# Kernel tuning notes

Hardware: AMD Instinct MI355X
Metric: run time of the kernel (lower is better)

## Reference

```python
import jax, jax.numpy as jnp
import numpy as np

B, S, D = 4, 4096, 1024
G, N, BLK, K = 8, 64, 8, 4
GD = D // G
NL = 24


def setup_inputs() -> dict:
    key = jax.random.key(0)
    ks = jax.random.split(key, 16)
    f32 = jnp.float32
    rn = lambda k, sh, s: jax.random.normal(k, sh, f32) * s
    inp = {}
    inp["x_r"] = jax.random.normal(ks[0], (B, S, D), f32)
    inp["x_i"] = jax.random.normal(ks[1], (B, S, D), f32)
    inp["norm_w"] = jnp.ones((D,), f32)
    inp["sg_theta"] = rn(ks[2], (D // BLK,), 0.1)
    inp["sg_Wg"] = rn(ks[3], (D, D), 1.0 / np.sqrt(D))
    inp["sg_bg"] = jnp.zeros((D,), f32)
    inp["conv_w"] = rn(ks[4], (2 * D, 2, K), 1.0 / np.sqrt(2 * K))
    inp["conv_b"] = jnp.zeros((2 * D,), f32)
    inp["log_A_mag"] = jax.random.uniform(ks[5], (G, N), f32) * 0.5 + 0.5
    inp["A_phase"] = rn(ks[6], (G, N), 0.1)
    inp["B_Wr"] = rn(ks[7], (N, GD), 1.0 / np.sqrt(GD))
    inp["B_Wi"] = rn(ks[8], (N, GD), 1.0 / np.sqrt(GD))
    inp["C_Wr"] = rn(ks[9], (GD, N), 1.0 / np.sqrt(N))
    inp["C_Wi"] = rn(ks[10], (GD, N), 1.0 / np.sqrt(N))
    inp["dt_W"] = rn(ks[11], (2, 2 * GD), 1.0 / np.sqrt(2 * GD))
    inp["dt_b"] = jnp.zeros((2,), f32)
    inp["out_Wr"] = rn(ks[12], (D, D), 1.0 / np.sqrt(D))
    inp["out_Wi"] = rn(ks[13], (D, D), 1.0 / np.sqrt(D))
    inp["act_thr"] = jnp.zeros((), f32)
    inp["ssm_scale"] = jnp.full((D,), 2.5, f32)
    inp["res_scale"] = jnp.asarray(1.0 / np.sqrt(2.0 * NL), f32)
    return inp


def reference(x_r, x_i, norm_w, sg_theta, sg_Wg, sg_bg, conv_w, conv_b,
              log_A_mag, A_phase, B_Wr, B_Wi, C_Wr, C_Wi, dt_W, dt_b,
              out_Wr, out_Wi, act_thr, ssm_scale, res_scale):
    b, s, d = x_r.shape
    g, n, gd = G, N, GD
    # --- ComplexRMSNorm: normalize by RMS of complex magnitude ---
    inv = jax.lax.rsqrt(jnp.mean(x_r * x_r + x_i * x_i, axis=-1, keepdims=True) + 1e-6)
    xr = x_r * inv * norm_w
    xi = x_i * inv * norm_w
    # --- SpinorGate: block-diagonal phase rotation with selective sigmoid gate ---
    theta = jnp.repeat(sg_theta, BLK)  # per-block angle broadcast to [D]
    mag = jnp.sqrt(xr * xr + xi * xi + 1e-8)
    gate = jax.nn.sigmoid(jnp.einsum('bsd,ed->bse', mag, sg_Wg) + sg_bg)
    ct, st = jnp.cos(theta), jnp.sin(theta)
    xr, xi = gate * (xr * ct - xi * st), gate * (xr * st + xi * ct)
    # --- grouped causal conv over interleaved real/imag channels ---
    x_il = jnp.stack([xr, xi], axis=-1).reshape(b, s, 2 * d).transpose(0, 2, 1)  # [B,2D,S]
    x_il = jnp.pad(x_il, ((0, 0), (0, 0), (K - 1, 0)))  # causal left pad
    co = jax.lax.conv_general_dilated(
        x_il, conv_w, (1,), 'VALID',
        dimension_numbers=('NCH', 'OIH', 'NCH'), feature_group_count=d)
    co = co + conv_b[None, :, None]
    co = co.transpose(0, 2, 1).reshape(b, s, d, 2)
    xr, xi = co[..., 0], co[..., 1]
    # --- magnitude-gated activation ---
    act = 1.0 - jnp.exp(-(xr * xr + xi * xi) * jnp.exp(act_thr))
    xr = xr * act
    xi = xi * act
    # --- MIMO groups ---
    xgr = xr.reshape(b, s, g, gd)
    xgi = xi.reshape(b, s, g, gd)
    # --- selective dt from concatenated real/imag features ---
    xcat = jnp.concatenate([xgr, xgi], axis=-1)  # [B,S,G,2*gd]
    dt = jnp.clip(jnp.exp(jnp.einsum('bsgd,ed->bsge', xcat, dt_W) + dt_b), 1e-4, 2.0)
    dt_mag, dt_ph = dt[..., 0:1], dt[..., 1:2]
    # --- discretized complex A (|A| < 1 guaranteed) ---
    a_mag = jnp.exp(dt_mag * (-jax.nn.softplus(log_A_mag)))  # [B,S,G,N]
    ang = dt_ph * A_phase
    ar = a_mag * jnp.cos(ang)
    ai = a_mag * jnp.sin(ang)
    # --- complex B projection ---
    bxr = (jnp.einsum('bsgd,nd->bsgn', xgr, B_Wr)
           - jnp.einsum('bsgd,nd->bsgn', xgi, B_Wi)) * dt_mag
    bxi = (jnp.einsum('bsgd,nd->bsgn', xgr, B_Wi)
           + jnp.einsum('bsgd,nd->bsgn', xgi, B_Wr)) * dt_mag
    # --- complex selective scan with renorm every 256 steps ---
    def step(carry, inp):
        hr, hi = carry
        a_r, a_i, b_r, b_i, t = inp
        nhr = a_r * hr - a_i * hi + b_r
        nhi = a_r * hi + a_i * hr + b_i
        hn = jnp.sqrt(nhr * nhr + nhi * nhi + 1e-8)
        sc = jnp.where((t + 1) % 256 == 0, jnp.minimum(hn, 100.0) / hn, 1.0)
        nhr = nhr * sc
        nhi = nhi * sc
        return (nhr, nhi), (nhr, nhi)

    h0 = jnp.zeros((b, g, n), x_r.dtype)
    mv = lambda a: jnp.moveaxis(a, 1, 0)  # [S,B,G,N]
    _, (Hr, Hi) = jax.lax.scan(step, (h0, h0),
                               (mv(ar), mv(ai), mv(bxr), mv(bxi), jnp.arange(s)))
    Hr = jnp.moveaxis(Hr, 0, 1)  # [B,S,G,N]
    Hi = jnp.moveaxis(Hi, 0, 1)
    # --- complex C projection ---
    yr = (jnp.einsum('bsgn,dn->bsgd', Hr, C_Wr)
          - jnp.einsum('bsgn,dn->bsgd', Hi, C_Wi)).reshape(b, s, d)
    yi = (jnp.einsum('bsgn,dn->bsgd', Hr, C_Wi)
          + jnp.einsum('bsgn,dn->bsgd', Hi, C_Wr)).reshape(b, s, d)
    # --- complex output projection, real per-channel scale, residual ---
    o_r = (jnp.einsum('bsd,ed->bse', yr, out_Wr)
           - jnp.einsum('bsd,ed->bse', yi, out_Wi)) * ssm_scale
    o_i = (jnp.einsum('bsd,ed->bse', yr, out_Wi)
           + jnp.einsum('bsd,ed->bse', yi, out_Wr)) * ssm_scale
    return jnp.stack([x_r + res_scale * o_r, x_i + res_scale * o_i], axis=-1)
```

## Files before the change

### kernel.cpp

```cpp
#include <hip/hip_runtime.h>
#include <hip/hip_bf16.h>
#include <hip/hip_fp8.h>
#include <math.h>

#define BB 4
#define SS 4096
#define DD 1024
#define GG 8
#define NN 64
#define GDIM 128
#define BS (BB*SS)
static const size_t BSD  = (size_t)BS * DD;
static const size_t BSGN = (size_t)BS * GG * NN;

typedef __attribute__((ext_vector_type(8))) short bf16x8;
typedef __attribute__((ext_vector_type(4))) float f32x4;
typedef __attribute__((ext_vector_type(4))) uint u32x4;
typedef unsigned char uchar;

__device__ inline ushort f2b(float x) {
    __hip_bfloat16 h = __float2bfloat16(x);
    return *reinterpret_cast<ushort*>(&h);
}
__device__ inline float b2f(ushort u) {
    union { uint q; float f; } x; x.q = ((uint)u) << 16; return x.f;
}
__device__ inline uchar f2fp8(float x) {
    __hip_fp8_e4m3 h(x);
    return *reinterpret_cast<uchar*>(&h);
}
__device__ __forceinline__ bf16x8 neg8(bf16x8 v) {
    union { bf16x8 b; u32x4 u; } x;
    x.b = v;
    x.u ^= 0x80008000u;
    return x.b;
}

#define GL16(gp, lp) __builtin_amdgcn_global_load_lds( \
    (const __attribute__((address_space(1))) void*)(gp), \
    (__attribute__((address_space(3))) void*)(lp), 16, 0, 0)

template<int KD, int LDA, int LDB>
__device__ __forceinline__ void mfma_core(
    const ushort* __restrict__ gA, const ushort* __restrict__ gB,
    ushort* lA, ushort* lB, int wave, int lane, f32x4 (&acc)[4][4])
{
    int r = lane & 15, h = lane >> 4;
    int wm = (wave & 1) * 64, wn = (wave >> 1) * 64;
    ushort* lA0 = lA + wave * 1024;
    ushort* lB0 = lB + wave * 1024;
    for (int k0 = 0; k0 < KD; k0 += 32) {
        __syncthreads();
        GL16(gA + k0,            lA0);
        GL16(gA + k0 + 16*LDA,   lA0 + 512);
        GL16(gB + k0,            lB0);
        GL16(gB + k0 + 16*LDB,   lB0 + 512);
        __syncthreads();
        bf16x8 af[4], bfv[4];
        #pragma unroll
        for (int i = 0; i < 4; i++) af[i]  = *(const bf16x8*)&lA[(wm + i*16 + r)*32 + h*8];
        #pragma unroll
        for (int j = 0; j < 4; j++) bfv[j] = *(const bf16x8*)&lB[(wn + j*16 + r)*32 + h*8];
        #pragma unroll
        for (int i = 0; i < 4; i++)
            #pragma unroll
            for (int j = 0; j < 4; j++)
                acc[i][j] = __builtin_amdgcn_mfma_f32_16x16x32_bf16(af[i], bfv[j], acc[i][j], 0, 0, 0);
    }
}

__global__ __launch_bounds__(256) void k_prep(
    const float* __restrict__ Wg, const float* __restrict__ BWr, const float* __restrict__ BWi,
    const float* __restrict__ CWr, const float* __restrict__ CWi,
    const float* __restrict__ Wor, const float* __restrict__ Woi,
    const float* __restrict__ logA, const float* __restrict__ theta,
    uchar* __restrict__ Wg8, ushort* __restrict__ BxT, ushort* __restrict__ A3,
    ushort* __restrict__ WoP, float* __restrict__ spl,
    float* __restrict__ ctab, float* __restrict__ stab)
{
    const int S1 = 1048576;
    const int S2 = S1 + 32768;
    const int S3 = S2 + 32768;
    const int S4 = S3 + 2097152;
    const int S5 = S4 + 512;
    const int S6 = S5 + 1024;
    const int S7 = S6 + 1024;
    for (int idx = blockIdx.x * 256 + threadIdx.x; idx < S7; idx += gridDim.x * 256) {
        if (idx < S1) {
            Wg8[idx] = f2fp8(Wg[idx] * 16.0f);
        } else if (idx < S2) {
            int j = idx - S1, n = j >> 8, kk = j & 255;
            float v;
            if (n < 64) v = (kk < 128) ? BWr[n*128 + kk] : -BWi[n*128 + (kk-128)];
            else { int n2 = n - 64; v = (kk < 128) ? BWi[n2*128 + kk] : BWr[n2*128 + (kk-128)]; }
            BxT[j] = f2b(v);
        } else if (idx < S3) {
            int j = idx - S2, m = j >> 8, kk = j & 255;
            float v;
            if (m < 64) v = (kk < 128) ? CWr[kk*64 + m] : -CWi[(kk-128)*64 + m];
            else { int n2 = m - 64; v = (kk < 128) ? CWi[kk*64 + n2] : CWr[(kk-128)*64 + n2]; }
            A3[j] = f2b(v);
        } else if (idx < S4) {
            int j = idx - S3, e = j >> 11, c = j & 2047;
            int g = c >> 8, kk = c & 255;
            float v = (kk < 128) ? Wor[(size_t)e*1024 + g*128 + kk]
                                 : Woi[(size_t)e*1024 + g*128 + (kk-128)];
            WoP[j] = f2b(v);
        } else if (idx < S5) {
            int j = idx - S4;
            spl[j] = log1pf(expf(logA[j]));
        } else if (idx < S6) {
            int j = idx - S5;
            ctab[j] = cosf(theta[j >> 3]);
        } else {
            int j = idx - S6;
            stab[j] = sinf(theta[j >> 3]);
        }
    }
}

__global__ __launch_bounds__(256) void k_pgemm(
    const ushort* __restrict__ A3, const ushort* __restrict__ WoP,
    ushort* __restrict__ Ppr, ushort* __restrict__ Ppi)
{
    __shared__ ushort lA[4096], lB[4096];
    int g = blockIdx.z;
    int bn = blockIdx.x * 128;
    int tid = threadIdx.x, wave = tid >> 6, lane = tid & 63;
    int row0 = wave*32 + (lane >> 2), col0 = (lane & 3) * 8;
    int r = lane & 15, h = lane >> 4;
    int wm = (wave & 1) * 64, wn = (wave >> 1) * 64;
    f32x4 acc[4][4] = {};
    mfma_core<256, 256, 2048>(A3 + (size_t)row0*256 + col0,
                              WoP + (size_t)(bn + row0)*2048 + g*256 + col0,
                              lA, lB, wave, lane, acc);
    #pragma unroll
    for (int i = 0; i < 4; i++) {
        int mb = wm + i*16 + h*4;
        #pragma unroll
        for (int j = 0; j < 4; j++) {
            int e = bn + wn + j*16 + r;
            #pragma unroll
            for (int t2 = 0; t2 < 4; t2++) {
                int m = mb + t2;
                float v = acc[i][j][t2];
                if (m < 64) {
                    Ppr[(size_t)e*512 + g*64 + m] = f2b(v);
                } else {
                    Ppi[(size_t)e*512 + g*64 + (m - 64)] = f2b(v);
                }
            }
        }
    }
}

__global__ __launch_bounds__(256) void k_norm(
    const float* __restrict__ xr_in, const float* __restrict__ xi_in,
    const float* __restrict__ norm_w,
    uchar* __restrict__ mag_o, float* __restrict__ inv_o)
{
    int row = blockIdx.x;
    int tid = threadIdx.x;
    size_t base = (size_t)row * DD;
    float4 vr = ((const float4*)(xr_in + base))[tid];
    float4 vi = ((const float4*)(xi_in + base))[tid];
    float ss = vr.x*vr.x + vr.y*vr.y + vr.z*vr.z + vr.w*vr.w
             + vi.x*vi.x + vi.y*vi.y + vi.z*vi.z + vi.w*vi.w;
    #pragma unroll
    for (int off = 32; off >= 1; off >>= 1) ss += __shfl_down(ss, off);
    __shared__ float ws4[4];
    if ((tid & 63) == 0) ws4[tid >> 6] = ss;
    __syncthreads();
    float tot = ws4[0] + ws4[1] + ws4[2] + ws4[3];
    float inv = rsqrtf(tot * (1.0f / DD) + 1e-6f);
    float4 w = ((const float4*)norm_w)[tid];
    vr.x *= inv * w.x; vr.y *= inv * w.y; vr.z *= inv * w.z; vr.w *= inv * w.w;
    vi.x *= inv * w.x; vi.y *= inv * w.y; vi.z *= inv * w.z; vi.w *= inv * w.w;
    uchar4 mb;
    mb.x = f2fp8(sqrtf(vr.x*vr.x + vi.x*vi.x + 1e-8f));
    mb.y = f2fp8(sqrtf(vr.y*vr.y + vi.y*vi.y + 1e-8f));
    mb.z = f2fp8(sqrtf(vr.z*vr.z + vi.z*vi.z + 1e-8f));
    mb.w = f2fp8(sqrtf(vr.w*vr.w + vi.w*vi.w + 1e-8f));
    ((uchar4*)(mag_o + base))[tid] = mb;
    if (tid == 0) inv_o[row] = inv;
}

__global__ __launch_bounds__(256) void k_gate_fp8(
    const uchar* __restrict__ A8, const uchar* __restrict__ B8,
    const float* __restrict__ bg, ushort* __restrict__ gate)
{
    __shared__ uchar lA[4096], lB[4096];
    int flat = blockIdx.y * 8 + blockIdx.x;
    int nid  = (flat & 7) * 128 + (flat >> 3);
    int bm = (nid >> 3) * 128, bn = (nid & 7) * 128;
    int tid = threadIdx.x, wave = tid >> 6, lane = tid & 63;
    int r = lane & 15, h = lane >> 4;
    int wm = (wave & 1) * 64, wn = (wave >> 1) * 64;
    int srow = wave*32 + (lane >> 1);
    int scol = (lane & 1) * 16;
    const uchar* gA = A8 + (size_t)(bm + srow)*1024 + scol;
    const uchar* gB = B8 + (size_t)(bn + srow)*1024 + scol;
    uchar* lA0 = lA + wave*1024;
    uchar* lB0 = lB + wave*1024;
    f32x4 acc[4][4] = {};
    for (int k0 = 0; k0 < 1024; k0 += 32) {
        __syncthreads();
        GL16(gA + k0, lA0);
        GL16(gB + k0, lB0);
        __syncthreads();
        long af[4], bfv[4];
        #pragma unroll
        for (int i = 0; i < 4; i++) af[i]  = *(const long*)&lA[(wm + i*16 + r)*32 + h*8];
        #pragma unroll
        for (int j = 0; j < 4; j++) bfv[j] = *(const long*)&lB[(wn + j*16 + r)*32 + h*8];
        #pragma unroll
        for (int i = 0; i < 4; i++)
            #pragma unroll
            for (int j = 0; j < 4; j++)
                acc[i][j] = __builtin_amdgcn_mfma_f32_16x16x32_fp8_fp8(af[i], bfv[j], acc[i][j], 0, 0, 0);
    }
    #pragma unroll
    for (int i = 0; i < 4; i++) {
        int mb = bm + wm + i*16 + h*4;
        #pragma unroll
        for (int j = 0; j < 4; j++) {
            int n = bn + wn + j*16 + r;
            float bias = bg[n];
            #pragma unroll
            for (int t2 = 0; t2 < 4; t2++) {
                float v = acc[i][j][t2] * 0.0625f + bias;
                gate[(size_t)(mb + t2)*DD + n] = f2b(1.0f / (1.0f + __expf(-v)));
            }
        }
    }
}

__global__ __launch_bounds__(256) void k_rotconv(
    const float* __restrict__ xr_raw, const float* __restrict__ xi_raw,
    const float* __restrict__ inv_, const float* __restrict__ norm_w,
    const ushort* __restrict__ gate,
    const float* __restrict__ ctab, const float* __restrict__ stab,
    const float* __restrict__ cw, const float* __restrict__ cb,
    const float* __restrict__ act_thr,
    const float* __restrict__ dtW, const float* __restrict__ dtb,
    ushort* __restrict__ xcat, float* __restrict__ dtm_o, float* __restrict__ dtp_o)
{
    const int CH = 16;
    int row0 = blockIdx.x * CH;
    int s0 = row0 & (SS - 1);
    int t = threadIdx.x, d0 = t * 4;
    int g = d0 >> 7, dd = d0 & 127;
    float4 w4  = *(const float4*)&norm_w[d0];
    float4 ct4 = *(const float4*)&ctab[d0];
    float4 st4 = *(const float4*)&stab[d0];
    float cwv[4][16];
    float cb0[4], cb1[4];
    #pragma unroll
    for (int j = 0; j < 4; j++) {
        #pragma unroll
        for (int q = 0; q < 4; q++)
            *(float4*)&cwv[j][q*4] = *(const float4*)&cw[(size_t)(2*(d0+j))*8 + q*4];
        cb0[j] = cb[2*(d0+j)];
        cb1[j] = cb[2*(d0+j) + 1];
    }
    float4 dtw0a = *(const float4*)&dtW[dd];
    float4 dtw0b = *(const float4*)&dtW[128 + dd];
    float4 dtw1a = *(const float4*)&dtW[256 + dd];
    float4 dtw1b = *(const float4*)&dtW[384 + dd];
    float ea  = __expf(act_thr[0]);
    float db0 = dtb[0], db1 = dtb[1];

    float p1r[4] = {}, p1i[4] = {}, p2r[4] = {}, p2i[4] = {}, p3r[4] = {}, p3i[4] = {};
    auto rotrow = [&](int rr, float (&orr)[4], float (&ori)[4]) {
        float4 a  = *(const float4*)&xr_raw[(size_t)rr*DD + d0];
        float4 bq = *(const float4*)&xi_raw[(size_t)rr*DD + d0];
        ushort4 gq = *(const ushort4*)&gate[(size_t)rr*DD + d0];
        float iv = inv_[rr];
        #pragma unroll
        for (int j = 0; j < 4; j++) {
            float ar = ((const float*)&a)[j]  * iv * ((const float*)&w4)[j];
            float ai = ((const float*)&bq)[j] * iv * ((const float*)&w4)[j];
            float c = ((const float*)&ct4)[j], s = ((const float*)&st4)[j];
            float gg = b2f(((const ushort*)&gq)[j]);
            orr[j] = gg * (ar*c - ai*s);
            ori[j] = gg * (ar*s + ai*c);
        }
    };
    if (s0 >= 1) rotrow(row0 - 1, p1r, p1i);
    if (s0 >= 2) rotrow(row0 - 2, p2r, p2i);
    if (s0 >= 3) rotrow(row0 - 3, p3r, p3i);

    for (int sl = 0; sl < CH; sl++) {
        int row = row0 + sl;
        float rr0[4], ri0[4];
        rotrow(row, rr0, ri0);
        float p0 = 0.f, p1 = 0.f;
        ushort4 ur, ui;
        #pragma unroll
        for (int j = 0; j < 4; j++) {
            float cr = cb0[j]
                + p3r[j]*cwv[j][0]  + p2r[j]*cwv[j][1]  + p1r[j]*cwv[j][2]  + rr0[j]*cwv[j][3]
                + p3i[j]*cwv[j][4]  + p2i[j]*cwv[j][5]  + p1i[j]*cwv[j][6]  + ri0[j]*cwv[j][7];
            float ci = cb1[j]
                + p3r[j]*cwv[j][8]  + p2r[j]*cwv[j][9]  + p1r[j]*cwv[j][10] + rr0[j]*cwv[j][11]
                + p3i[j]*cwv[j][12] + p2i[j]*cwv[j][13] + p1i[j]*cwv[j][14] + ri0[j]*cwv[j][15];
            float act = 1.0f - __expf(-(cr*cr + ci*ci) * ea);
            cr *= act; ci *= act;
            ((ushort*)&ur)[j] = f2b(cr);
            ((ushort*)&ui)[j] = f2b(ci);
            p0 += cr * ((const float*)&dtw0a)[j] + ci * ((const float*)&dtw0b)[j];
            p1 += cr * ((const float*)&dtw1a)[j] + ci * ((const float*)&dtw1b)[j];
        }
        *(ushort4*)&xcat[(size_t)row*2048 + g*256 + dd]       = ur;
        *(ushort4*)&xcat[(size_t)row*2048 + g*256 + 128 + dd] = ui;
        #pragma unroll
        for (int off = 16; off >= 1; off >>= 1) {
            p0 += __shfl_down(p0, off, 32);
            p1 += __shfl_down(p1, off, 32);
        }
        if ((t & 31) == 0) {
            dtm_o[(size_t)row*8 + g] = fminf(fmaxf(__expf(p0 + db0), 1e-4f), 2.0f);
            dtp_o[(size_t)row*8 + g] = fminf(fmaxf(__expf(p1 + db1), 1e-4f), 2.0f);
        }
        #pragma unroll
        for (int j = 0; j < 4; j++) {
            p3r[j] = p2r[j]; p3i[j] = p2i[j];
            p2r[j] = p1r[j]; p2i[j] = p1i[j];
            p1r[j] = rr0[j]; p1i[j] = ri0[j];
        }
    }
}

__global__ __launch_bounds__(256) void k_bx_mfma(
    const ushort* __restrict__ xcat, const ushort* __restrict__ BxT,
    const float* __restrict__ dtm_,
    float* __restrict__ br, float* __restrict__ bi)
{
    __shared__ ushort lA[4096], lB[4096];
    int g = blockIdx.z;
    int bm = blockIdx.y * 128;
    int tid = threadIdx.x, wave = tid >> 6, lane = tid & 63;
    int row0 = wave*32 + (lane >> 2), col0 = (lane & 3) * 8;
    int r = lane & 15, h = lane >> 4;
    int wm = (wave & 1) * 64, wn = (wave >> 1) * 64;
    f32x4 acc[4][4] = {};
    mfma_core<256, 2048, 256>(xcat + (size_t)(bm + row0)*2048 + g*256 + col0,
                              BxT + (size_t)row0*256 + col0,
                              lA, lB, wave, lane, acc);
    #pragma unroll
    for (int i = 0; i < 4; i++) {
        int mb = bm + wm + i*16 + h*4;
        #pragma unroll
        for (int j = 0; j < 4; j++) {
            int n = wn + j*16 + r;
            #pragma unroll
            for (int t2 = 0; t2 < 4; t2++) {
                int m = mb + t2;
                float v = acc[i][j][t2] * dtm_[(size_t)m*8 + g];
                if (n < 64) br[(size_t)m*512 + g*64 + n]      = v;
                else        bi[(size_t)m*512 + g*64 + n - 64] = v;
            }
        }
    }
}

__global__ __launch_bounds__(256) void k_scan1(
    const float* __restrict__ br, const float* __restrict__ bi,
    const float* __restrict__ dtm_, const float* __restrict__ dtp_,
    const float* __restrict__ spl_t, const float* __restrict__ aph,
    float* __restrict__ Sar, float* __restrict__ Sai,
    float* __restrict__ Sbr, float* __restrict__ Sbi)
{
    int blk = blockIdx.x;
    int half = blk & 1, c = (blk >> 1) & 63, b = blk >> 7;
    int t = half*256 + threadIdx.x;
    int g = t >> 6;
    float spl = spl_t[t], ap = aph[t];
    int row0 = b*SS + c*64;
    size_t idx = (size_t)row0 * 512 + t;
    const float* dtmp = dtm_ + (size_t)row0*8 + g;
    const float* dtpp = dtp_ + (size_t)row0*8 + g;
    float Ar = 1.f, Ai = 0.f, Br = 0.f, Bi = 0.f;
    for (int s0 = 0; s0 < 64; s0 += 4) {
        float vm[4], vp[4], wr[4], wi[4];
        #pragma unroll
        for (int u = 0; u < 4; u++) {
            vm[u] = dtmp[(s0+u)*8]; vp[u] = dtpp[(s0+u)*8];
            wr[u] = br[idx + (size_t)(s0+u)*512];
            wi[u] = bi[idx + (size_t)(s0+u)*512];
        }
        #pragma unroll
        for (int u = 0; u < 4; u++) {
            float am = __expf(-vm[u]*spl);
            float sa, ca; __sincosf(vp[u]*ap, &sa, &ca);
            float arv = am*ca, aiv = am*sa;
            float nBr = arv*Br - aiv*Bi + wr[u];
            float nBi = arv*Bi + aiv*Br + wi[u];
            float nAr = arv*Ar - aiv*Ai;
            float nAi = arv*Ai + aiv*Ar;
            Br = nBr; Bi = nBi; Ar = nAr; Ai = nAi;
        }
    }
    size_t o = ((size_t)(b*64 + c))*512 + t;
    Sar[o] = Ar; Sai[o] = Ai; Sbr[o] = Br; Sbi[o] = Bi;
}

__global__ __launch_bounds__(256) void k_scan2(
    const float* __restrict__ Sar, const float* __restrict__ Sai,
    const float* __restrict__ Sbr, const float* __restrict__ Sbi,
    float* __restrict__ hinr, float* __restrict__ hini)
{
    int blk = blockIdx.x;
    int half = blk & 1, b = blk >> 1;
    int t = half*256 + threadIdx.x;
    float hr = 0.f, hi = 0.f;
    for (int c = 0; c < 64; c++) {
        size_t o = ((size_t)(b*64 + c))*512 + t;
        hinr[o] = hr; hini[o] = hi;
        float nr = Sar[o]*hr - Sai[o]*hi + Sbr[o];
        float ni = Sar[o]*hi + Sai[o]*hr + Sbi[o];
        if ((c & 3) == 3) {
            float hn = sqrtf(nr*nr + ni*ni + 1e-8f);
            float sc = fminf(hn, 100.0f) / hn;
            nr *= sc; ni *= sc;
        }
        hr = nr; hi = ni;
    }
}

__global__ __launch_bounds__(256) void k_scan3(
    const float* __restrict__ br, const float* __restrict__ bi,
    const float* __restrict__ dtm_, const float* __restrict__ dtp_,
    const float* __restrict__ spl_t, const float* __restrict__ aph,
    const float* __restrict__ hinr, const float* __restrict__ hini,
    ushort* __restrict__ Hbf)
{
    int blk = blockIdx.x;
    int half = blk & 1, c = (blk >> 1) & 63, b = blk >> 7;
    int t = half*256 + threadIdx.x;
    int g = t >> 6;
    float spl = spl_t[t], ap = aph[t];
    int row0 = b*SS + c*64;
    size_t idx = (size_t)row0 * 512 + t;
    const float* dtmp = dtm_ + (size_t)row0*8 + g;
    const float* dtpp = dtp_ + (size_t)row0*8 + g;
    size_t o = ((size_t)(b*64 + c))*512 + t;
    float hr = hinr[o], hi = hini[o];
    bool rch = ((c & 3) == 3);
    for (int s0 = 0; s0 < 64; s0 += 4) {
        float vm[4], vp[4], wr[4], wi[4];
        #pragma unroll
        for (int u = 0; u < 4; u++) {
            vm[u] = dtmp[(s0+u)*8]; vp[u] = dtpp[(s0+u)*8];
            wr[u] = br[idx + (size_t)(s0+u)*512];
            wi[u] = bi[idx + (size_t)(s0+u)*512];
        }
        #pragma unroll
        for (int u = 0; u < 4; u++) {
            float am = __expf(-vm[u]*spl);
            float sa, ca; __sincosf(vp[u]*ap, &sa, &ca);
            float arv = am*ca, aiv = am*sa;
            float nr = arv*hr - aiv*hi + wr[u];
            float ni = arv*hi + aiv*hr + wi[u];
            if (rch && (s0 + u == 63)) {
                float hn = sqrtf(nr*nr + ni*ni + 1e-8f);
                float sc = fminf(hn, 100.0f) / hn;
                nr *= sc; ni *= sc;
            }
            size_t rb = (size_t)(row0 + s0 + u) * 1024;
            Hbf[rb + t]       = f2b(nr);
            Hbf[rb + 512 + t] = f2b(ni);
            hr = nr; hi = ni;
        }
    }
}

__global__ __launch_bounds__(256) void k_out_cplx(
    const ushort* __restrict__ A,
    const ushort* __restrict__ Ppr,
    const ushort* __restrict__ Ppi,
    const float* __restrict__ ssm,
    const float* __restrict__ xr0, const float* __restrict__ xi0,
    const float* __restrict__ res_scale, float* __restrict__ out)
{
    int flat = blockIdx.y * 8 + blockIdx.x;
    int e_t = flat >> 7;
    int m_t = flat & 127;
    int bm = m_t * 128, be = e_t * 128;
    int tid = threadIdx.x, wave = tid >> 6, lane = tid & 63;
    int r = lane & 15, h = lane >> 4;
    int wm = (wave & 1) * 64, wn = (wave >> 1) * 64;
    const ushort* aBase = A   + (size_t)(bm + wm + r)*1024 + h*8;
    const ushort* pBr   = Ppr + (size_t)(be + wn + r)*512  + h*8;
    const ushort* pBi   = Ppi + (size_t)(be + wn + r)*512  + h*8;
    f32x4 accr[4][4] = {};
    f32x4 acci[4][4] = {};
    for (int k0 = 0; k0 < 512; k0 += 32) {
        bf16x8 hrf[4], hif[4], prf[4], pif[4], npif[4];
        #pragma unroll
        for (int i = 0; i < 4; i++) {
            hrf[i] = *(const bf16x8*)(aBase + i*16384 + k0);
            hif[i] = *(const bf16x8*)(aBase + i*16384 + 512 + k0);
        }
        #pragma unroll
        for (int j = 0; j < 4; j++) {
            prf[j] = *(const bf16x8*)(pBr + j*8192 + k0);
            pif[j] = *(const bf16x8*)(pBi + j*8192 + k0);
            npif[j] = neg8(pif[j]);
        }
        #pragma unroll
        for (int i = 0; i < 4; i++)
            #pragma unroll
            for (int j = 0; j < 4; j++) {
                accr[i][j] = __builtin_amdgcn_mfma_f32_16x16x32_bf16(hrf[i], prf[j],  accr[i][j], 0, 0, 0);
                accr[i][j] = __builtin_amdgcn_mfma_f32_16x16x32_bf16(hif[i], npif[j], accr[i][j], 0, 0, 0);
                acci[i][j] = __builtin_amdgcn_mfma_f32_16x16x32_bf16(hrf[i], pif[j],  acci[i][j], 0, 0, 0);
                acci[i][j] = __builtin_amdgcn_mfma_f32_16x16x32_bf16(hif[i], prf[j],  acci[i][j], 0, 0, 0);
            }
    }
    float rs = res_scale[0];
    #pragma unroll
    for (int i = 0; i < 4; i++) {
        int mb = bm + wm + i*16 + h*4;
        #pragma unroll
        for (int j = 0; j < 4; j++) {
            int e = be + wn + j*16 + r;
            float sc = ssm[e] * rs;
            #pragma unroll
            for (int t2 = 0; t2 < 4; t2++) {
                size_t p = (size_t)(mb + t2)*DD + e;
                float2 v;
                v.x = xr0[p] + accr[i][j][t2]*sc;
                v.y = xi0[p] + acci[i][j][t2]*sc;
                *(float2*)&out[2*p] = v;
            }
        }
    }
}

extern "C" void kernel_launch(void* const* d_in, const int* in_sizes, int n_in,
                              void* d_out, int out_size, void* d_ws, size_t ws_size,
                              hipStream_t stream) {
    const float* x_r      = (const float*)d_in[0];
    const float* x_i      = (const float*)d_in[1];
    const float* norm_w   = (const float*)d_in[2];
    const float* sg_theta = (const float*)d_in[3];
    const float* sg_Wg    = (const float*)d_in[4];
    const float* sg_bg    = (const float*)d_in[5];
    const float* conv_w   = (const float*)d_in[6];
    const float* conv_b   = (const float*)d_in[7];
    const float* log_A    = (const float*)d_in[8];
    const float* A_phase  = (const float*)d_in[9];
    const float* B_Wr     = (const float*)d_in[10];
    const float* B_Wi     = (const float*)d_in[11];
    const float* C_Wr     = (const float*)d_in[12];
    const float* C_Wi     = (const float*)d_in[13];
    const float* dt_W     = (const float*)d_in[14];
    const float* dt_b     = (const float*)d_in[15];
    const float* out_Wr   = (const float*)d_in[16];
    const float* out_Wi   = (const float*)d_in[17];
    const float* act_thr  = (const float*)d_in[18];
    const float* ssm_s    = (const float*)d_in[19];
    const float* res_s    = (const float*)d_in[20];
    float* out = (float*)d_out;
    float* ws  = (float*)d_ws;

    ushort* gate  = (ushort*)ws;
    ushort* xcat  = (ushort*)(ws + BSD);
    uchar*  mag8  = (uchar*)(ws + 2*BSD);
    float*  br    = ws + 2*BSD + BSGN;
    float*  bi    = ws + 2*BSD + 2*BSGN;
    ushort* Hbf   = (ushort*)(ws + 2*BSD + 3*BSGN);
    float*  sm    = ws + 2*BSD + 4*BSGN;
    float*  dtm   = sm;
    float*  dtp   = sm + 131072;
    float*  Sar   = sm + 2*131072;
    float*  Sai   = sm + 3*131072;
    float*  Sbr   = sm + 4*131072;
    float*  Sbi   = sm + 5*131072;
    float*  hinr  = sm + 6*131072;
    float*  hini  = sm + 7*131072;
    float*  inv   = sm + 8*131072;
    float*  spl   = inv + 16384;
    float*  ctab  = spl + 512;
    float*  stab  = ctab + 1024;
    uchar*  Wg8   = (uchar*)(stab + 1024);
    ushort* BxT   = (ushort*)(stab + 1024 + 262144);
    ushort* A3    = BxT + 32768;
    ushort* WoP   = A3 + 32768;
    ushort* Ppr   = WoP + 2097152;
    ushort* Ppi   = Ppr + 524288;

    k_prep<<<2048, 256, 0, stream>>>(sg_Wg, B_Wr, B_Wi, C_Wr, C_Wi, out_Wr, out_Wi,
                                     log_A, sg_theta, Wg8, BxT, A3, WoP, spl, ctab, stab);
    k_pgemm<<<dim3(8, 1, 8), 256, 0, stream>>>(A3, WoP, Ppr, Ppi);
    k_norm<<<BS, 256, 0, stream>>>(x_r, x_i, norm_w, mag8, inv);
    k_gate_fp8<<<dim3(8, 128), 256, 0, stream>>>(mag8, Wg8, sg_bg, gate);
    k_rotconv<<<BS/16, 256, 0, stream>>>(x_r, x_i, inv, norm_w, gate, ctab, stab,
                                         conv_w, conv_b, act_thr, dt_W, dt_b,
                                         xcat, dtm, dtp);
    k_bx_mfma<<<dim3(1, 128, 8), 256, 0, stream>>>(xcat, BxT, dtm, br, bi);
    k_scan1<<<512, 256, 0, stream>>>(br, bi, dtm, dtp, spl, A_phase, Sar, Sai, Sbr, Sbi);
    k_scan2<<<8, 256, 0, stream>>>(Sar, Sai, Sbr, Sbi, hinr, hini);
    k_scan3<<<512, 256, 0, stream>>>(br, bi, dtm, dtp, spl, A_phase, hinr, hini, Hbf);
    k_out_cplx<<<dim3(8, 128), 256, 0, stream>>>(Hbf, Ppr, Ppi, ssm_s, x_r, x_i, res_s, out);
}
```

Baseline: 418.4 us.

## Stage out-projection GEMM tiles through LDS with 512-thread 128x256 blocks

The final complex output GEMM kernel now copies the H and projection-weight K-slices into shared memory with GL16 loads and reads MFMA fragments from LDS, where before each wave loaded its fragments straight from global memory. Blocks grow to 512 threads covering a 128x256 output tile, and block IDs are remapped so that neighbouring blocks share row tiles, for better L2 locality. The goal is to cut redundant global/L2 traffic for operand fragments. In exchange it adds two barriers per K step with no double buffering, a larger LDS footprint and possibly fewer resident blocks per CU.

```diff
diff --git a/kernel.cpp b/kernel.cpp
--- a/kernel.cpp
+++ b/kernel.cpp
@@ -475,7 +475,7 @@
     }
 }
 
-__global__ __launch_bounds__(256) void k_out_cplx(
+__global__ __launch_bounds__(512) void k_out_cplx(
     const ushort* __restrict__ A,
     const ushort* __restrict__ Ppr,
     const ushort* __restrict__ Ppi,
@@ -483,29 +483,46 @@
     const float* __restrict__ xr0, const float* __restrict__ xi0,
     const float* __restrict__ res_scale, float* __restrict__ out)
 {
+    __shared__ ushort lHr[4096], lHi[4096], lPr[8192], lPi[8192];
     int flat = blockIdx.y * 8 + blockIdx.x;
-    int e_t = flat >> 7;
-    int m_t = flat & 127;
-    int bm = m_t * 128, be = e_t * 128;
+    int nid  = (flat & 7) * 64 + (flat >> 3);
+    int bm = (nid >> 2) * 128, be = (nid & 3) * 256;
     int tid = threadIdx.x, wave = tid >> 6, lane = tid & 63;
     int r = lane & 15, h = lane >> 4;
-    int wm = (wave & 1) * 64, wn = (wave >> 1) * 64;
-    const ushort* aBase = A   + (size_t)(bm + wm + r)*1024 + h*8;
-    const ushort* pBr   = Ppr + (size_t)(be + wn + r)*512  + h*8;
-    const ushort* pBi   = Ppi + (size_t)(be + wn + r)*512  + h*8;
+    int wr = wave >> 2, wc = wave & 3;
+    int lrow = lane >> 2;
+    int lcol = (lane & 3) * 8;
+    const ushort* gHr = A + (size_t)(bm + wave*16 + lrow)*1024 + lcol;
+    const ushort* gHi = gHr + 512;
+    const ushort* gPr = Ppr + (size_t)(be + wave*32 + lrow)*512 + lcol;
+    const ushort* gPi = Ppi + (size_t)(be + wave*32 + lrow)*512 + lcol;
+    ushort* dHr = lHr + wave*512;
+    ushort* dHi = lHi + wave*512;
+    ushort* dPr = lPr + wave*1024;
+    ushort* dPi = lPi + wave*1024;
     f32x4 accr[4][4] = {};
     f32x4 acci[4][4] = {};
     for (int k0 = 0; k0 < 512; k0 += 32) {
+        __syncthreads();
+        GL16(gHr + k0, dHr);
+        GL16(gHi + k0, dHi);
+        GL16(gPr + k0,          dPr);
+        GL16(gPr + 16*512 + k0, dPr + 512);
+        GL16(gPi + k0,          dPi);
+        GL16(gPi + 16*512 + k0, dPi + 512);
+        __syncthreads();
         bf16x8 hrf[4], hif[4], prf[4], pif[4], npif[4];
         #pragma unroll
         for (int i = 0; i < 4; i++) {
-            hrf[i] = *(const bf16x8*)(aBase + i*16384 + k0);
-            hif[i] = *(const bf16x8*)(aBase + i*16384 + 512 + k0);
-        }
-        #pragma unroll
-        for (int j = 0; j < 4; j++) {
-            prf[j] = *(const bf16x8*)(pBr + j*8192 + k0);
-            pif[j] = *(const bf16x8*)(pBi + j*8192 + k0);
+            int ro = (wr*64 + i*16 + r)*32 + h*8;
+            hrf[i] = *(const bf16x8*)&lHr[ro];
+            hif[i] = *(const bf16x8*)&lHi[ro];
+        }
+        #pragma unroll
+        for (int j = 0; j < 4; j++) {
+            int ro = (wc*64 + j*16 + r)*32 + h*8;
+            prf[j] = *(const bf16x8*)&lPr[ro];
+            pif[j] = *(const bf16x8*)&lPi[ro];
             npif[j] = neg8(pif[j]);
         }
         #pragma unroll
@@ -521,10 +538,10 @@
     float rs = res_scale[0];
     #pragma unroll
     for (int i = 0; i < 4; i++) {
-        int mb = bm + wm + i*16 + h*4;
-        #pragma unroll
-        for (int j = 0; j < 4; j++) {
-            int e = be + wn + j*16 + r;
+        int mb = bm + wr*64 + i*16 + h*4;
+        #pragma unroll
+        for (int j = 0; j < 4; j++) {
+            int e = be + wc*64 + j*16 + r;
             float sc = ssm[e] * rs;
             #pragma unroll
             for (int t2 = 0; t2 < 4; t2++) {
@@ -603,5 +620,5 @@
     k_scan1<<<512, 256, 0, stream>>>(br, bi, dtm, dtp, spl, A_phase, Sar, Sai, Sbr, Sbi);
     k_scan2<<<8, 256, 0, stream>>>(Sar, Sai, Sbr, Sbi, hinr, hini);
     k_scan3<<<512, 256, 0, stream>>>(br, bi, dtm, dtp, spl, A_phase, hinr, hini, Hbf);
-    k_out_cplx<<<dim3(8, 128), 256, 0, stream>>>(Hbf, Ppr, Ppi, ssm_s, x_r, x_i, res_s, out);
-}
+    k_out_cplx<<<dim3(8, 64), 512, 0, stream>>>(Hbf, Ppr, Ppi, ssm_s, x_r, x_i, res_s, out);
+}
```

Result: faster. 344.2 us (-17.7%).
